# Kernel optimization log

Measured on AMD Instinct MI355X. Metric: run time of the kernel, lower is better.

Reference implementation:

```python
import jax, jax.numpy as jnp
import numpy as np

B, E, K, S, D, H, C = 8192, 8, 2, 32, 3072, 256, 100  # batch, experts, fix_points, img size, flat dim, hidden, classes


def setup_inputs() -> dict:
    key = jax.random.key(0)
    ks = jax.random.split(key, 6)
    return {
        "x": jax.random.normal(ks[0], (B, 3, S, S), jnp.float32),
        "coeffs_t": jax.random.uniform(ks[1], (K,), jnp.float32),
        "router_w": jax.random.normal(ks[2], (K, D, E), jnp.float32) * 0.02,
        "router_b": jnp.zeros((K, E), jnp.float32),
        "w1": jax.random.normal(ks[3], (E, K, D, H), jnp.float32) * 0.02,
        "b1": jnp.zeros((E, K, H), jnp.float32),
        "w2": jax.random.normal(ks[4], (E, K, H, C), jnp.float32) * 0.02,
        "b2": jnp.zeros((E, K, C), jnp.float32),
    }


def reference(x, coeffs_t, router_w, router_b, w1, b1, w2, b2):
    xf = x.reshape(x.shape[0], -1)  # [B, D]
    # Curve parameter blend: W = sum_k coeffs_t[k] * W_k (CurveParameter semantics)
    Wr = jnp.einsum('k,kde->de', coeffs_t, router_w)
    br = jnp.einsum('k,ke->e', coeffs_t, router_b)
    # Router: top-1 expert index per sample
    idx = jnp.argmax(xf @ Wr + br, axis=-1)  # [B] int
    # Blended expert weights
    W1 = jnp.einsum('k,ekdh->edh', coeffs_t, w1)
    B1 = jnp.einsum('k,ekh->eh', coeffs_t, b1)
    W2 = jnp.einsum('k,ekhc->ehc', coeffs_t, w2)
    B2 = jnp.einsum('k,ekc->ec', coeffs_t, b2)
    # Expert MLP (computed for all experts with static shapes, then top-1 gather;
    # identical math to torch's boolean-mask dispatch/scatter)
    h = jax.nn.gelu(jnp.einsum('bd,edh->beh', xf, W1) + B1, approximate=False)  # [B,E,H]
    o = jnp.einsum('beh,ehc->bec', h, W2) + B2  # [B,E,C]
    return jnp.take_along_axis(o, idx[:, None, None], axis=1)[:, 0, :]  # [B,C]
```

## Files before the change

### kernel.cpp

```cpp
#include <hip/hip_runtime.h>
#include <math.h>

#define B_  8192
#define E_  8
#define D_  3072
#define H_  256
#define C_  100
#define DH_ (D_*H_)
#define HC_ (H_*C_)
#define KS_ 8
#define KSEG_ (D_/KS_)
#define RKS_ 16
#define RSEG_ (D_/RKS_)
#define RB_ (B_/256)
#define NTMAX_ 136
#define NT2MAX_ 528

#define MEGA_R_   (RB_*RKS_)
#define MEGA_W1_  (24*4*8)
#define MEGA_W2_  (C_*E_)
#define MEGA_BB_  3
#define MEGA_TOT_ (MEGA_R_ + MEGA_W1_ + MEGA_W2_ + MEGA_BB_)

typedef __attribute__((ext_vector_type(4))) float  f32x4;
typedef __attribute__((ext_vector_type(8))) __bf16 bf16x8;
typedef __attribute__((ext_vector_type(8))) unsigned short ush8;
typedef __attribute__((ext_vector_type(4))) unsigned short ush4;

__device__ inline unsigned short bf16_rne(float f) {
    unsigned u = __builtin_bit_cast(unsigned, f);
    unsigned r = (u + 0x7FFFu + ((u >> 16) & 1u)) >> 16;
    return (unsigned short)r;
}
__device__ inline float bf16_f(unsigned short h) {
    unsigned u = ((unsigned)h) << 16;
    return __builtin_bit_cast(float, u);
}

#define MISC_B1_ (E_*H_/4)
#define MISC_B2_ (E_*C_/4)

__global__ __launch_bounds__(256) void mega_k(
        const float* __restrict__ x, const float* __restrict__ rw,
        const float* __restrict__ w1, const float* __restrict__ w2,
        const float* __restrict__ b1, const float* __restrict__ b2,
        unsigned short* __restrict__ Whi, unsigned short* __restrict__ Wlo,
        unsigned short* __restrict__ W2thi, unsigned short* __restrict__ W2tlo,
        float* __restrict__ B1b, float* __restrict__ B2b,
        double* __restrict__ lpart, const float* __restrict__ coeffs) {
    __shared__ char smem[36864];
    int bid = blockIdx.x;
    int t = threadIdx.x;

    if (bid < MEGA_R_) {
        float  (*xs)[64][33] = (float(*)[64][33])smem;
        double (*wls)[8]     = (double(*)[8])(smem + 33792);
        int w = t >> 6, lane = t & 63;
        int rowblk = (bid & (RB_ - 1)) * 256;
        int s2     = bid >> 5;
        int kbase  = s2 * RSEG_;
        int row0   = rowblk + w * 64;
        double c0 = (double)coeffs[0], c1 = (double)coeffs[1];

        double acc[8] = {0, 0, 0, 0, 0, 0, 0, 0};

        for (int kb = 0; kb < RSEG_; kb += 32) {
            #pragma unroll
            for (int it = 0; it < 8; it++) {
                int i = lane + it * 64;
                int r = i >> 3, c4 = i & 7;
                *(float4*)&xs[w][r][c4 * 4] =
                    *(const float4*)(x + (size_t)(row0 + r) * D_ + kbase + kb + c4 * 4);
            }
            if (w == 0) {
                #pragma unroll
                for (int it = 0; it < 4; it++) {
                    int i = lane + it * 64;
                    int k = i >> 3, ee = i & 7;
                    wls[k][ee] = c0 * (double)rw[(size_t)(kbase + kb + k) * 8 + ee]
                               + c1 * (double)rw[(size_t)(D_ + kbase + kb + k) * 8 + ee];
                }
            }
            __syncthreads();
            #pragma unroll
            for (int kk = 0; kk < 32; kk++) {
                double xv = (double)xs[w][lane][kk];
                double2 w01 = *(const double2*)&wls[kk][0];
                double2 w23 = *(const double2*)&wls[kk][2];
                double2 w45 = *(const double2*)&wls[kk][4];
                double2 w67 = *(const double2*)&wls[kk][6];
                acc[0] = fma(xv, w01.x, acc[0]);
                acc[1] = fma(xv, w01.y, acc[1]);
                acc[2] = fma(xv, w23.x, acc[2]);
                acc[3] = fma(xv, w23.y, acc[3]);
                acc[4] = fma(xv, w45.x, acc[4]);
                acc[5] = fma(xv, w45.y, acc[5]);
                acc[6] = fma(xv, w67.x, acc[6]);
                acc[7] = fma(xv, w67.y, acc[7]);
            }
            __syncthreads();
        }
        size_t base = ((size_t)s2 * B_ + row0 + lane) * 8;
        #pragma unroll
        for (int ee = 0; ee < 8; ee++) lpart[base + ee] = acc[ee];

    } else if (bid < MEGA_R_ + MEGA_W1_) {
        int lid = bid - MEGA_R_;
        int e  = lid / 96;
        int r  = lid - e * 96;
        int h0 = (r / 24) * 64;
        int d0 = (r % 24) * 128;
        const int TP = 136;
        unsigned short* thi = (unsigned short*)smem;
        unsigned short* tlo = thi + 64 * TP;
        float c0 = coeffs[0], c1 = coeffs[1];
        int h = t & 63, dl = t >> 6;
        const float* pa = w1 + ((size_t)(e * 2 + 0) * D_ + d0) * H_ + h0 + h;
        const float* pb = w1 + ((size_t)(e * 2 + 1) * D_ + d0) * H_ + h0 + h;
        for (int it = 0; it < 32; it++) {
            int d = it * 4 + dl;
            float v = c0 * pa[(size_t)d * H_] + c1 * pb[(size_t)d * H_];
            unsigned short hi = bf16_rne(v);
            thi[h * TP + d] = hi;
            tlo[h * TP + d] = bf16_rne(v - bf16_f(hi));
        }
        __syncthreads();
        #pragma unroll
        for (int it = 0; it < 4; it++) {
            int i = t + it * 256;
            int hh = i >> 4, d8 = (i & 15) * 8;
            size_t g = (size_t)(e * H_ + h0 + hh) * D_ + d0 + d8;
            *(ush8*)(Whi + g) = *(const ush8*)&thi[hh * TP + d8];
            *(ush8*)(Wlo + g) = *(const ush8*)&tlo[hh * TP + d8];
        }

    } else if (bid < MEGA_R_ + MEGA_W1_ + MEGA_W2_) {
        int lid = bid - (MEGA_R_ + MEGA_W1_);
        int c = lid % C_, e = lid / C_;
        int k = t;
        float c0 = coeffs[0], c1 = coeffs[1];
        float v = c0 * w2[((size_t)(e * 2 + 0) * H_ + k) * C_ + c]
                + c1 * w2[((size_t)(e * 2 + 1) * H_ + k) * C_ + c];
        unsigned short hi = bf16_rne(v);
        W2thi[(size_t)(e * C_ + c) * H_ + k] = hi;
        W2tlo[(size_t)(e * C_ + c) * H_ + k] = bf16_rne(v - bf16_f(hi));

    } else {
        int gid = (bid - (MEGA_R_ + MEGA_W1_ + MEGA_W2_)) * 256 + t;
        float c0 = coeffs[0], c1 = coeffs[1];
        if (gid < MISC_B1_) {
            const float4* p = (const float4*)b1;
            int e = gid / (H_ / 4), r = gid - e * (H_ / 4);
            float4 a = p[(e * 2 + 0) * (H_ / 4) + r];
            float4 bq = p[(e * 2 + 1) * (H_ / 4) + r];
            float4 o;
            o.x = c0 * a.x + c1 * bq.x;
            o.y = c0 * a.y + c1 * bq.y;
            o.z = c0 * a.z + c1 * bq.z;
            o.w = c0 * a.w + c1 * bq.w;
            ((float4*)B1b)[gid] = o;
        } else if (gid < MISC_B1_ + MISC_B2_) {
            int g2 = gid - MISC_B1_;
            const float4* p = (const float4*)b2;
            int e = g2 / (C_ / 4), r = g2 - e * (C_ / 4);
            float4 a = p[(e * 2 + 0) * (C_ / 4) + r];
            float4 bq = p[(e * 2 + 1) * (C_ / 4) + r];
            float4 o;
            o.x = c0 * a.x + c1 * bq.x;
            o.y = c0 * a.y + c1 * bq.y;
            o.z = c0 * a.z + c1 * bq.z;
            o.w = c0 * a.w + c1 * bq.w;
            ((float4*)B2b)[g2] = o;
        }
    }
}

__global__ __launch_bounds__(256) void argmax_k(
        const double* __restrict__ lpart, const float* __restrict__ rb,
        const float* __restrict__ coeffs, int* __restrict__ idx,
        int* __restrict__ cnt) {
    __shared__ int scnt[8];
    int t = threadIdx.x;
    if (t < 8) scnt[t] = 0;
    __syncthreads();
    int b = blockIdx.x * 256 + t;
    double c0 = (double)coeffs[0], c1 = (double)coeffs[1];
    double l[8];
    #pragma unroll
    for (int e = 0; e < 8; e++)
        l[e] = c0 * (double)rb[e] + c1 * (double)rb[8 + e];
    for (int s2 = 0; s2 < RKS_; s2++) {
        const double2* pp = (const double2*)(lpart + ((size_t)s2 * B_ + b) * 8);
        double2 v0 = pp[0], v1 = pp[1], v2 = pp[2], v3 = pp[3];
        l[0] += v0.x; l[1] += v0.y; l[2] += v1.x; l[3] += v1.y;
        l[4] += v2.x; l[5] += v2.y; l[6] += v3.x; l[7] += v3.y;
    }
    double best = -1e300;
    int bi = 0;
    #pragma unroll
    for (int e = 0; e < 8; e++)
        if (l[e] > best) { best = l[e]; bi = e; }
    idx[b] = bi;
    atomicAdd(&scnt[bi], 1);
    __syncthreads();
    if (t < 8 && scnt[t] > 0) atomicAdd(&cnt[t], scnt[t]);
}

__global__ void offsets_k(const int* __restrict__ cnt, int* __restrict__ off,
                          int* __restrict__ cursor, int* __restrict__ tmap,
                          int* __restrict__ tmap2, int* __restrict__ ntl) {
    if (threadIdx.x == 0) {
        int s = 0;
        for (int e = 0; e < E_; e++) { off[e] = s; cursor[e] = s; s += cnt[e]; }
        int nt = 0;
        for (int e = 0; e < E_; e++)
            for (int t0 = 0; t0 < cnt[e]; t0 += 64)
                tmap[nt++] = (e << 16) | t0;
        ntl[0] = nt;
        int nt2 = 0;
        for (int e = 0; e < E_; e++)
            for (int t0 = 0; t0 < cnt[e]; t0 += 16)
                tmap2[nt2++] = (e << 16) | t0;
        ntl[1] = nt2;
    }
}

__global__ void scatter_k(const int* __restrict__ idx, int* __restrict__ cursor,
                          int* __restrict__ order) {
    int b = blockIdx.x * blockDim.x + threadIdx.x;
    if (b < B_) {
        int e = idx[b];
        int pos = atomicAdd(&cursor[e], 1);
        order[pos] = (e << 16) | b;
    }
}

template<int MODE>
__global__ __launch_bounds__(256, 3) void gemm1_t(
        const float* __restrict__ x, const unsigned short* __restrict__ Whi,
        const unsigned short* __restrict__ Wlo, const int* __restrict__ order,
        const int* __restrict__ cnt, const int* __restrict__ off,
        const int* __restrict__ tmap, const int* __restrict__ ntl,
        float* __restrict__ dst) {
    int tid = blockIdx.y;
    if (tid >= ntl[0]) return;
    int tm = tmap[tid];
    int e = tm >> 16, tile0 = tm & 0xFFFF;
    int ce = cnt[e];
    int s = blockIdx.x;

    __shared__ int rows[64];
    __shared__ unsigned short xs_hi[64 * 40];
    __shared__ unsigned short xs_lo[64 * 40];
    __shared__ unsigned short ws_hi[256 * 40];
    __shared__ unsigned short ws_lo[256 * 40];

    int t = threadIdx.x;
    if (t < 64) {
        int i = tile0 + t;
        rows[t] = (i < ce) ? (order[off[e] + i] & 0xFFFF) : -1;
    }
    __syncthreads();
    int xrow0 = rows[0];

    int lane = t & 63, w = t >> 6;
    int lr = lane & 15, quad = lane >> 4;
    int kbase = s * KSEG_;

    f32x4 acc[4][4];
    #pragma unroll
    for (int mt = 0; mt < 4; mt++)
        #pragma unroll
        for (int nt = 0; nt < 4; nt++)
            acc[mt][nt] = (f32x4){0.f, 0.f, 0.f, 0.f};

    for (int kb = 0; kb < KSEG_; kb += 32) {
        #pragma unroll
        for (int it = 0; it < 2; it++) {
            int i = t + it * 256;
            int rr = i >> 3, sg = i & 7;
            int row = rows[rr];
            if (row < 0) row = xrow0;
            float4 v = *(const float4*)(x + (size_t)row * D_ + kbase + kb + sg * 4);
            unsigned short h4[4], l4[4];
            float vv[4] = {v.x, v.y, v.z, v.w};
            #pragma unroll
            for (int j = 0; j < 4; j++) {
                unsigned short hi = bf16_rne(vv[j]);
                h4[j] = hi;
                l4[j] = bf16_rne(vv[j] - bf16_f(hi));
            }
            *(ush4*)&xs_hi[rr * 40 + sg * 4] = *(const ush4*)h4;
            *(ush4*)&xs_lo[rr * 40 + sg * 4] = *(const ush4*)l4;
        }
        #pragma unroll
        for (int it = 0; it < 4; it++) {
            int i = t + it * 256;
            int col = i >> 2, ch = i & 3;
            size_t g = (size_t)(e * H_ + col) * D_ + kbase + kb + ch * 8;
            *(ush8*)&ws_hi[col * 40 + ch * 8] = *(const ush8*)(Whi + g);
            *(ush8*)&ws_lo[col * 40 + ch * 8] = *(const ush8*)(Wlo + g);
        }
        __syncthreads();

        bf16x8 ah[4], al[4], bh[4], bl[4];
        #pragma unroll
        for (int mt = 0; mt < 4; mt++) {
            ah[mt] = __builtin_bit_cast(bf16x8, *(const ush8*)&xs_hi[(mt * 16 + lr) * 40 + quad * 8]);
            al[mt] = __builtin_bit_cast(bf16x8, *(const ush8*)&xs_lo[(mt * 16 + lr) * 40 + quad * 8]);
        }
        #pragma unroll
        for (int nt = 0; nt < 4; nt++) {
            int col = w * 64 + nt * 16 + lr;
            bh[nt] = __builtin_bit_cast(bf16x8, *(const ush8*)&ws_hi[col * 40 + quad * 8]);
            bl[nt] = __builtin_bit_cast(bf16x8, *(const ush8*)&ws_lo[col * 40 + quad * 8]);
        }
        #pragma unroll
        for (int mt = 0; mt < 4; mt++)
            #pragma unroll
            for (int nt = 0; nt < 4; nt++) {
                acc[mt][nt] = __builtin_amdgcn_mfma_f32_16x16x32_bf16(ah[mt], bh[nt], acc[mt][nt], 0, 0, 0);
                acc[mt][nt] = __builtin_amdgcn_mfma_f32_16x16x32_bf16(al[mt], bh[nt], acc[mt][nt], 0, 0, 0);
                acc[mt][nt] = __builtin_amdgcn_mfma_f32_16x16x32_bf16(ah[mt], bl[nt], acc[mt][nt], 0, 0, 0);
                acc[mt][nt] = __builtin_amdgcn_mfma_f32_16x16x32_bf16(al[mt], bl[nt], acc[mt][nt], 0, 0, 0);
            }
        __syncthreads();
    }

    size_t p0 = (size_t)off[e] + tile0;
    if (MODE == 1) {
        float* dp = dst + ((size_t)s * B_ + p0) * H_;
        #pragma unroll
        for (int mt = 0; mt < 4; mt++) {
            int rl = mt * 16 + quad * 4;
            #pragma unroll
            for (int nt = 0; nt < 4; nt++) {
                int col = w * 64 + nt * 16 + lr;
                #pragma unroll
                for (int rg = 0; rg < 4; rg++) {
                    if (tile0 + rl + rg < ce)
                        dp[(size_t)(rl + rg) * H_ + col] = acc[mt][nt][rg];
                }
            }
        }
    } else {
        #pragma unroll
        for (int mt = 0; mt < 4; mt++) {
            int rl = mt * 16 + quad * 4;
            #pragma unroll
            for (int nt = 0; nt < 4; nt++) {
                int col = w * 64 + nt * 16 + lr;
                #pragma unroll
                for (int rg = 0; rg < 4; rg++) {
                    if (tile0 + rl + rg < ce)
                        atomicAdd(&dst[(p0 + rl + rg) * H_ + col], acc[mt][nt][rg]);
                }
            }
        }
    }
}

__global__ __launch_bounds__(256) void bias_gelu_k(
        float* __restrict__ hws, const float* __restrict__ B1b,
        const int* __restrict__ order) {
    int gid = blockIdx.x * 256 + threadIdx.x;
    int p = gid >> 6, c4 = (gid & 63) * 4;
    int e = order[p] >> 16;
    float4 v = *(const float4*)(hws + (size_t)p * H_ + c4);
    const float4 bb = *(const float4*)(B1b + e * H_ + c4);
    float pre[4] = {v.x + bb.x, v.y + bb.y, v.z + bb.z, v.w + bb.w};
    float4 o;
    o.x = 0.5f * pre[0] * (1.0f + erff(pre[0] * 0.70710678118654752440f));
    o.y = 0.5f * pre[1] * (1.0f + erff(pre[1] * 0.70710678118654752440f));
    o.z = 0.5f * pre[2] * (1.0f + erff(pre[2] * 0.70710678118654752440f));
    o.w = 0.5f * pre[3] * (1.0f + erff(pre[3] * 0.70710678118654752440f));
    *(float4*)(hws + (size_t)p * H_ + c4) = o;
}

template<int FUSE>
__global__ __launch_bounds__(256) void gemm2_t(
        const float* __restrict__ hsrc,
        const unsigned short* __restrict__ W2thi, const unsigned short* __restrict__ W2tlo,
        const float* __restrict__ B1b, const float* __restrict__ B2b,
        const int* __restrict__ order, const int* __restrict__ cnt,
        const int* __restrict__ off, const int* __restrict__ tmap2,
        const int* __restrict__ ntl, float* __restrict__ out) {
    int tid = blockIdx.x;
    if (tid >= ntl[1]) return;
    int tm = tmap2[tid];
    int e = tm >> 16, tile0 = tm & 0xFFFF;
    int ce = cnt[e];

    __shared__ int rows[16];
    __shared__ float red[3][64][28];

    int t = threadIdx.x;
    if (t < 16) {
        int i = tile0 + t;
        rows[t] = (i < ce) ? (order[off[e] + i] & 0xFFFF) : -1;
    }
    __syncthreads();

    int lane = t & 63, w = t >> 6;
    int m = lane & 15, q = lane >> 4;
    int p = off[e] + tile0 + ((tile0 + m < ce) ? m : 0);

    f32x4 acc[7];
    #pragma unroll
    for (int nt = 0; nt < 7; nt++) acc[nt] = (f32x4){0.f, 0.f, 0.f, 0.f};

    const unsigned short* w2h = W2thi + (size_t)e * C_ * H_;
    const unsigned short* w2l = W2tlo + (size_t)e * C_ * H_;

    #pragma unroll
    for (int si = 0; si < 2; si++) {
        int s = w * 2 + si;
        int k0 = s * 32 + q * 8;
        size_t o = (size_t)p * H_ + k0;
        float f[8];
        if (FUSE) {
            float4 a0 = *(const float4*)(hsrc + o);
            float4 a1 = *(const float4*)(hsrc + o + 4);
            #pragma unroll
            for (int s2 = 1; s2 < KS_; s2++) {
                const float* sp = hsrc + (size_t)s2 * B_ * H_ + o;
                float4 b0 = *(const float4*)sp;
                float4 b1v = *(const float4*)(sp + 4);
                a0.x += b0.x; a0.y += b0.y; a0.z += b0.z; a0.w += b0.w;
                a1.x += b1v.x; a1.y += b1v.y; a1.z += b1v.z; a1.w += b1v.w;
            }
            float4 bb0 = *(const float4*)(B1b + e * H_ + k0);
            float4 bb1 = *(const float4*)(B1b + e * H_ + k0 + 4);
            float pre[8] = {a0.x + bb0.x, a0.y + bb0.y, a0.z + bb0.z, a0.w + bb0.w,
                            a1.x + bb1.x, a1.y + bb1.y, a1.z + bb1.z, a1.w + bb1.w};
            #pragma unroll
            for (int j = 0; j < 8; j++)
                f[j] = 0.5f * pre[j] * (1.0f + erff(pre[j] * 0.70710678118654752440f));
        } else {
            float4 v0 = *(const float4*)(hsrc + o);
            float4 v1 = *(const float4*)(hsrc + o + 4);
            f[0] = v0.x; f[1] = v0.y; f[2] = v0.z; f[3] = v0.w;
            f[4] = v1.x; f[5] = v1.y; f[6] = v1.z; f[7] = v1.w;
        }
        unsigned short hh[8], lo[8];
        #pragma unroll
        for (int j = 0; j < 8; j++) {
            unsigned short hi = bf16_rne(f[j]);
            hh[j] = hi;
            lo[j] = bf16_rne(f[j] - bf16_f(hi));
        }
        bf16x8 ah = __builtin_bit_cast(bf16x8, *(const ush8*)hh);
        bf16x8 al = __builtin_bit_cast(bf16x8, *(const ush8*)lo);
        #pragma unroll
        for (int nt = 0; nt < 7; nt++) {
            size_t bo = (size_t)(nt * 16 + m) * H_ + k0;
            bf16x8 bh = __builtin_bit_cast(bf16x8, *(const ush8*)(w2h + bo));
            bf16x8 bl = __builtin_bit_cast(bf16x8, *(const ush8*)(w2l + bo));
            acc[nt] = __builtin_amdgcn_mfma_f32_16x16x32_bf16(ah, bh, acc[nt], 0, 0, 0);
            acc[nt] = __builtin_amdgcn_mfma_f32_16x16x32_bf16(al, bh, acc[nt], 0, 0, 0);
            acc[nt] = __builtin_amdgcn_mfma_f32_16x16x32_bf16(ah, bl, acc[nt], 0, 0, 0);
            acc[nt] = __builtin_amdgcn_mfma_f32_16x16x32_bf16(al, bl, acc[nt], 0, 0, 0);
        }
    }

    if (w > 0) {
        #pragma unroll
        for (int nt = 0; nt < 7; nt++)
            #pragma unroll
            for (int i = 0; i < 4; i++)
                red[w - 1][lane][nt * 4 + i] = acc[nt][i];
    }
    __syncthreads();
    if (w == 0) {
        #pragma unroll
        for (int nt = 0; nt < 7; nt++)
            #pragma unroll
            for (int i = 0; i < 4; i++)
                acc[nt][i] = ((acc[nt][i] + red[0][lane][nt * 4 + i])
                              + red[1][lane][nt * 4 + i]) + red[2][lane][nt * 4 + i];
        #pragma unroll
        for (int nt = 0; nt < 7; nt++) {
            int c = nt * 16 + m;
            if (c >= C_) continue;
            float bias = B2b[e * C_ + c];
            #pragma unroll
            for (int i = 0; i < 4; i++) {
                int grow = q * 4 + i;
                if (tile0 + grow < ce)
                    out[(size_t)rows[grow] * C_ + c] = acc[nt][i] + bias;
            }
        }
    }
}

extern "C" void kernel_launch(void* const* d_in, const int* in_sizes, int n_in,
                              void* d_out, int out_size, void* d_ws, size_t ws_size,
                              hipStream_t stream) {
    const float* x        = (const float*)d_in[0];
    const float* coeffs   = (const float*)d_in[1];
    const float* router_w = (const float*)d_in[2];
    const float* router_b = (const float*)d_in[3];
    const float* w1       = (const float*)d_in[4];
    const float* b1       = (const float*)d_in[5];
    const float* w2       = (const float*)d_in[6];
    const float* b2       = (const float*)d_in[7];
    float* out = (float*)d_out;

    unsigned short* Whi   = (unsigned short*)d_ws;
    unsigned short* Wlo   = Whi + (size_t)E_ * DH_;
    unsigned short* W2thi = Wlo + (size_t)E_ * DH_;
    unsigned short* W2tlo = W2thi + (size_t)E_ * C_ * H_;
    float* B1b  = (float*)(W2tlo + (size_t)E_ * C_ * H_);
    float* B2b  = B1b + (size_t)E_ * H_;
    int* order  = (int*)(B2b + E_ * C_);
    int* cnt    = order + B_;
    int* off    = cnt + E_;
    int* cursor = off + E_;
    int* tmap   = cursor + E_;
    int* tmap2  = tmap + NTMAX_;
    int* ntl    = tmap2 + NT2MAX_;
    int* idx    = ntl + 4;
    float* hws  = (float*)(idx + B_);
    double* lpart = (double*)hws;

    size_t prefix_bytes = (size_t)((char*)hws - (char*)d_ws);
    int use_part = (ws_size >= prefix_bytes + (size_t)KS_ * B_ * H_ * sizeof(float) + 256) ? 1 : 0;

    hipMemsetAsync(cnt, 0, 3 * E_ * sizeof(int), stream);

    mega_k<<<dim3(MEGA_TOT_), 256, 0, stream>>>(
        x, router_w, w1, w2, b1, b2, Whi, Wlo, W2thi, W2tlo, B1b, B2b,
        lpart, coeffs);

    argmax_k<<<dim3(B_ / 256), 256, 0, stream>>>(lpart, router_b, coeffs, idx, cnt);
    offsets_k<<<1, 64, 0, stream>>>(cnt, off, cursor, tmap, tmap2, ntl);
    scatter_k<<<dim3(B_ / 256), 256, 0, stream>>>(idx, cursor, order);

    if (use_part) {
        gemm1_t<1><<<dim3(KS_, NTMAX_), 256, 0, stream>>>(x, Whi, Wlo, order, cnt,
                                                          off, tmap, ntl, hws);
        gemm2_t<1><<<dim3(NT2MAX_), 256, 0, stream>>>(hws, W2thi, W2tlo, B1b, B2b,
                                                      order, cnt, off, tmap2, ntl, out);
    } else {
        hipMemsetAsync(hws, 0, (size_t)B_ * H_ * sizeof(float), stream);
        gemm1_t<0><<<dim3(KS_, NTMAX_), 256, 0, stream>>>(x, Whi, Wlo, order, cnt,
                                                          off, tmap, ntl, hws);
        bias_gelu_k<<<dim3(B_ * H_ / 4 / 256), 256, 0, stream>>>(hws, B1b, order);
        gemm2_t<0><<<dim3(NT2MAX_), 256, 0, stream>>>(hws, W2thi, W2tlo, B1b, B2b,
                                                      order, cnt, off, tmap2, ntl, out);
    }
}
```

Baseline: 358.8 us.

## Fuse routing offsets into scatter, prefetch router inputs into registers

New measurement: 344.5 us. 1.04x faster.

```diff
diff --git a/kernel.cpp b/kernel.cpp
--- a/kernel.cpp
+++ b/kernel.cpp
@@ -64,24 +64,60 @@
 
         double acc[8] = {0, 0, 0, 0, 0, 0, 0, 0};
 
+        float4 px[8];
+        float rwa[4], rwb[4];
+        #pragma unroll
+        for (int it = 0; it < 8; it++) {
+            int i = lane + it * 64;
+            int r = i >> 3, c4 = i & 7;
+            px[it] = *(const float4*)(x + (size_t)(row0 + r) * D_ + kbase + c4 * 4);
+        }
+        if (w == 0) {
+            #pragma unroll
+            for (int it = 0; it < 4; it++) {
+                int i = lane + it * 64;
+                int k = i >> 3, ee = i & 7;
+                rwa[it] = rw[(size_t)(kbase + k) * 8 + ee];
+                rwb[it] = rw[(size_t)(D_ + kbase + k) * 8 + ee];
+            }
+        }
+
         for (int kb = 0; kb < RSEG_; kb += 32) {
             #pragma unroll
             for (int it = 0; it < 8; it++) {
                 int i = lane + it * 64;
                 int r = i >> 3, c4 = i & 7;
-                *(float4*)&xs[w][r][c4 * 4] =
-                    *(const float4*)(x + (size_t)(row0 + r) * D_ + kbase + kb + c4 * 4);
+                *(float4*)&xs[w][r][c4 * 4] = px[it];
             }
             if (w == 0) {
                 #pragma unroll
                 for (int it = 0; it < 4; it++) {
                     int i = lane + it * 64;
                     int k = i >> 3, ee = i & 7;
-                    wls[k][ee] = c0 * (double)rw[(size_t)(kbase + kb + k) * 8 + ee]
-                               + c1 * (double)rw[(size_t)(D_ + kbase + kb + k) * 8 + ee];
+                    wls[k][ee] = c0 * (double)rwa[it] + c1 * (double)rwb[it];
                 }
             }
             __syncthreads();
+
+            if (kb + 32 < RSEG_) {
+                #pragma unroll
+                for (int it = 0; it < 8; it++) {
+                    int i = lane + it * 64;
+                    int r = i >> 3, c4 = i & 7;
+                    px[it] = *(const float4*)(x + (size_t)(row0 + r) * D_ +
+                                              kbase + kb + 32 + c4 * 4);
+                }
+                if (w == 0) {
+                    #pragma unroll
+                    for (int it = 0; it < 4; it++) {
+                        int i = lane + it * 64;
+                        int k = i >> 3, ee = i & 7;
+                        rwa[it] = rw[(size_t)(kbase + kb + 32 + k) * 8 + ee];
+                        rwb[it] = rw[(size_t)(D_ + kbase + kb + 32 + k) * 8 + ee];
+                    }
+                }
+            }
+
             #pragma unroll
             for (int kk = 0; kk < 32; kk++) {
                 double xv = (double)xs[w][lane][kk];
@@ -117,6 +153,7 @@
         int h = t & 63, dl = t >> 6;
         const float* pa = w1 + ((size_t)(e * 2 + 0) * D_ + d0) * H_ + h0 + h;
         const float* pb = w1 + ((size_t)(e * 2 + 1) * D_ + d0) * H_ + h0 + h;
+        #pragma unroll 8
         for (int it = 0; it < 32; it++) {
             int d = it * 4 + dl;
             float v = c0 * pa[(size_t)d * H_] + c1 * pb[(size_t)d * H_];
@@ -175,10 +212,10 @@
     }
 }
 
-__global__ __launch_bounds__(256) void argmax_k(
+__global__ __launch_bounds__(256) void argmax_hist_k(
         const double* __restrict__ lpart, const float* __restrict__ rb,
         const float* __restrict__ coeffs, int* __restrict__ idx,
-        int* __restrict__ cnt) {
+        int* __restrict__ hist) {
     __shared__ int scnt[8];
     int t = threadIdx.x;
     if (t < 8) scnt[t] = 0;
@@ -203,35 +240,57 @@
     idx[b] = bi;
     atomicAdd(&scnt[bi], 1);
     __syncthreads();
-    if (t < 8 && scnt[t] > 0) atomicAdd(&cnt[t], scnt[t]);
-}
-
-__global__ void offsets_k(const int* __restrict__ cnt, int* __restrict__ off,
-                          int* __restrict__ cursor, int* __restrict__ tmap,
-                          int* __restrict__ tmap2, int* __restrict__ ntl) {
-    if (threadIdx.x == 0) {
+    if (t < 8) hist[blockIdx.x * 8 + t] = scnt[t];
+}
+
+__global__ __launch_bounds__(256) void scatter2_k(
+        const int* __restrict__ idx, const int* __restrict__ hist,
+        int* __restrict__ order, int* __restrict__ cnt, int* __restrict__ off,
+        int* __restrict__ tmap, int* __restrict__ tmap2, int* __restrict__ ntl) {
+    __shared__ int sbi[256];
+    __shared__ int stot[8];
+    __shared__ int sbase[8];
+    int b0 = blockIdx.x, t = threadIdx.x;
+    int b = b0 * 256 + t;
+    int mybi = idx[b];
+    sbi[t] = mybi;
+    if (t < 8) {
+        int tot = 0, pre = 0;
+        for (int bb = 0; bb < RB_; bb++) {
+            int h = hist[bb * 8 + t];
+            if (bb < b0) pre += h;
+            tot += h;
+        }
+        stot[t] = tot;
+        sbase[t] = pre;
+    }
+    __syncthreads();
+    if (t < 8) {
+        int o = 0;
+        for (int j = 0; j < t; j++) o += stot[j];
+        sbase[t] += o;
+    }
+    __syncthreads();
+    int rank = 0;
+    for (int i = 0; i < 256; i++) {
+        int v = sbi[i];
+        rank += (i < t && v == mybi) ? 1 : 0;
+    }
+    order[sbase[mybi] + rank] = (mybi << 16) | b;
+
+    if (b0 == 0 && t == 0) {
         int s = 0;
-        for (int e = 0; e < E_; e++) { off[e] = s; cursor[e] = s; s += cnt[e]; }
+        for (int e = 0; e < E_; e++) { cnt[e] = stot[e]; off[e] = s; s += stot[e]; }
         int nt = 0;
         for (int e = 0; e < E_; e++)
-            for (int t0 = 0; t0 < cnt[e]; t0 += 64)
+            for (int t0 = 0; t0 < stot[e]; t0 += 64)
                 tmap[nt++] = (e << 16) | t0;
         ntl[0] = nt;
         int nt2 = 0;
         for (int e = 0; e < E_; e++)
-            for (int t0 = 0; t0 < cnt[e]; t0 += 16)
+            for (int t0 = 0; t0 < stot[e]; t0 += 16)
                 tmap2[nt2++] = (e << 16) | t0;
         ntl[1] = nt2;
-    }
-}
-
-__global__ void scatter_k(const int* __restrict__ idx, int* __restrict__ cursor,
-                          int* __restrict__ order) {
-    int b = blockIdx.x * blockDim.x + threadIdx.x;
-    if (b < B_) {
-        int e = idx[b];
-        int pos = atomicAdd(&cursor[e], 1);
-        order[pos] = (e << 16) | b;
     }
 }
 
@@ -515,26 +574,24 @@
     int* order  = (int*)(B2b + E_ * C_);
     int* cnt    = order + B_;
     int* off    = cnt + E_;
-    int* cursor = off + E_;
-    int* tmap   = cursor + E_;
+    int* tmap   = off + E_;
     int* tmap2  = tmap + NTMAX_;
     int* ntl    = tmap2 + NT2MAX_;
     int* idx    = ntl + 4;
-    float* hws  = (float*)(idx + B_);
+    int* hist   = idx + B_;
+    float* hws  = (float*)(hist + 256);
     double* lpart = (double*)hws;
 
     size_t prefix_bytes = (size_t)((char*)hws - (char*)d_ws);
     int use_part = (ws_size >= prefix_bytes + (size_t)KS_ * B_ * H_ * sizeof(float) + 256) ? 1 : 0;
-
-    hipMemsetAsync(cnt, 0, 3 * E_ * sizeof(int), stream);
 
     mega_k<<<dim3(MEGA_TOT_), 256, 0, stream>>>(
         x, router_w, w1, w2, b1, b2, Whi, Wlo, W2thi, W2tlo, B1b, B2b,
         lpart, coeffs);
 
-    argmax_k<<<dim3(B_ / 256), 256, 0, stream>>>(lpart, router_b, coeffs, idx, cnt);
-    offsets_k<<<1, 64, 0, stream>>>(cnt, off, cursor, tmap, tmap2, ntl);
-    scatter_k<<<dim3(B_ / 256), 256, 0, stream>>>(idx, cursor, order);
+    argmax_hist_k<<<dim3(RB_), 256, 0, stream>>>(lpart, router_b, coeffs, idx, hist);
+    scatter2_k<<<dim3(RB_), 256, 0, stream>>>(idx, hist, order, cnt, off,
+                                              tmap, tmap2, ntl);
 
     if (use_part) {
         gemm1_t<1><<<dim3(KS_, NTMAX_), 256, 0, stream>>>(x, Whi, Wlo, order, cnt,
```
